# Performance work log

Hardware: AMD Instinct MI355X
Metric: run time of the kernel (lower is better)

## Reference

```python
import jax, jax.numpy as jnp
import numpy as np


def setup_inputs() -> dict:
    key = jax.random.key(0)
    k1, = jax.random.split(key, 1)
    x = jax.random.normal(k1, (8, 256, 128, 128), dtype=jnp.float32)
    alpha = jnp.ones((1,), dtype=jnp.float32)
    return {"x": x, "alpha": alpha}


def reference(x, alpha):
    B, C, H, W = x.shape
    v = x.reshape(B, C, H * W)                 # [B, C, HW] (query=key=value)
    energy = jnp.einsum('bcs,bds->bcd', v, v)  # [B, C, C]
    # max-softmax: softmax(max(energy) - energy) along last dim
    energy_new = jnp.max(energy, axis=-1, keepdims=True) - energy
    w = jax.nn.softmax(energy_new, axis=-1)    # [B, C, C]
    y = jnp.einsum('bcd,bds->bcs', w, v)       # [B, C, HW]
    y = y.reshape(B, C, H, W)
    return alpha * y + x
```

## Files before the change

### kernel.cpp

```cpp
#include <hip/hip_runtime.h>
#include <math.h>

static constexpr int Bn = 8;
static constexpr int Cn = 256;
static constexpr int Sn = 16384;

typedef __bf16 bf16x4 __attribute__((ext_vector_type(4)));
typedef __bf16 bf16x8 __attribute__((ext_vector_type(8)));
typedef float  f32x4  __attribute__((ext_vector_type(4)));

static constexpr int TILE   = 128;
static constexpr int KB     = 32;
static constexpr int KSPLIT = 16;
static constexpr int KSLICE = Sn / KSPLIT;

__device__ __forceinline__ void split_store(__bf16* __restrict__ Hi, __bf16* __restrict__ Lo,
                                            int row, int kq, float4 v) {
  __bf16 h0 = (__bf16)v.x, h1 = (__bf16)v.y, h2 = (__bf16)v.z, h3 = (__bf16)v.w;
  int off = row * 32 + (((kq >> 1) ^ (row & 3)) << 3) + ((kq & 1) << 2);
  *(bf16x4*)&Hi[off] = (bf16x4){h0, h1, h2, h3};
  *(bf16x4*)&Lo[off] = (bf16x4){(__bf16)(v.x - (float)h0), (__bf16)(v.y - (float)h1),
                                (__bf16)(v.z - (float)h2), (__bf16)(v.w - (float)h3)};
}

__device__ __forceinline__ bf16x8 frag_ld(const __bf16* __restrict__ P, int row, int quad) {
  return *(const bf16x8*)&P[row * 32 + ((quad ^ (row & 3)) << 3)];
}

__global__ __launch_bounds__(256, 2) void gram_part_kernel(const float* __restrict__ x,
                                                           float* __restrict__ P) {
  const int b    = blockIdx.z;
  const int tsel = blockIdx.y;
  const int kk   = blockIdx.x;
  const int ti   = (tsel == 1) ? 1 : 0;
  const int tj   = (tsel == 0) ? 0 : 1;
  const bool diag = (tsel < 2);

  const float* vb    = x + (size_t)b * Cn * Sn;
  const float* Abase = vb + (size_t)(ti * TILE) * Sn + kk * KSLICE;
  const float* Bbase = vb + (size_t)(tj * TILE) * Sn + kk * KSLICE;

  __shared__ __align__(16) __bf16 Ah[TILE * 32];
  __shared__ __align__(16) __bf16 Al[TILE * 32];
  __shared__ __align__(16) __bf16 Bh[TILE * 32];
  __shared__ __align__(16) __bf16 Bl[TILE * 32];

  const int t    = threadIdx.x;
  const int lane = t & 63;
  const int wv   = t >> 6;
  const int wr   = wv >> 1;
  const int wc   = wv & 1;
  const int ln   = lane & 15;
  const int quad = lane >> 4;
  const int srow = t >> 3;
  const int skq  = t & 7;

  float4 areg[4], breg[4];
#pragma unroll
  for (int it = 0; it < 4; it++)
    areg[it] = *(const float4*)(Abase + (size_t)(srow + it * 32) * Sn + skq * 4);
  if (!diag) {
#pragma unroll
    for (int it = 0; it < 4; it++)
      breg[it] = *(const float4*)(Bbase + (size_t)(srow + it * 32) * Sn + skq * 4);
  }

  f32x4 acc[4][4];
#pragma unroll
  for (int i = 0; i < 4; i++)
#pragma unroll
    for (int j = 0; j < 4; j++) acc[i][j] = (f32x4){0.f, 0.f, 0.f, 0.f};

  for (int kc = 0; kc < KSLICE; kc += KB) {
#pragma unroll
    for (int it = 0; it < 4; it++) split_store(Ah, Al, srow + it * 32, skq, areg[it]);
    if (!diag) {
#pragma unroll
      for (int it = 0; it < 4; it++) split_store(Bh, Bl, srow + it * 32, skq, breg[it]);
    }
    __syncthreads();

    const __bf16* PH = diag ? Ah : Bh;
    const __bf16* PL = diag ? Al : Bl;

    bf16x8 fah[4], fal[4];
#pragma unroll
    for (int i = 0; i < 4; i++) {
      int ar = wr * 64 + i * 16 + ln;
      fah[i] = frag_ld(Ah, ar, quad);
      fal[i] = frag_ld(Al, ar, quad);
    }

    if (kc + KB < KSLICE) {
#pragma unroll
      for (int it = 0; it < 4; it++)
        areg[it] = *(const float4*)(Abase + (size_t)(srow + it * 32) * Sn + (kc + KB) + skq * 4);
      if (!diag) {
#pragma unroll
        for (int it = 0; it < 4; it++)
          breg[it] = *(const float4*)(Bbase + (size_t)(srow + it * 32) * Sn + (kc + KB) + skq * 4);
      }
    }

#pragma unroll
    for (int j = 0; j < 4; j++) {
      int br = wc * 64 + j * 16 + ln;
      bf16x8 fbh = frag_ld(PH, br, quad);
      bf16x8 fbl = frag_ld(PL, br, quad);
#pragma unroll
      for (int i = 0; i < 4; i++) {
        acc[i][j] = __builtin_amdgcn_mfma_f32_16x16x32_bf16(fah[i], fbh, acc[i][j], 0, 0, 0);
        acc[i][j] = __builtin_amdgcn_mfma_f32_16x16x32_bf16(fah[i], fbl, acc[i][j], 0, 0, 0);
        acc[i][j] = __builtin_amdgcn_mfma_f32_16x16x32_bf16(fal[i], fbh, acc[i][j], 0, 0, 0);
      }
    }
    __syncthreads();
  }

  float* Pb = P + ((size_t)kk * Bn + b) * (Cn * Cn);
#pragma unroll
  for (int i = 0; i < 4; i++)
#pragma unroll
    for (int j = 0; j < 4; j++) {
      int c0 = ti * TILE + wr * 64 + i * 16 + quad * 4;
      int d  = tj * TILE + wc * 64 + j * 16 + ln;
#pragma unroll
      for (int r = 0; r < 4; r++) {
        float v = acc[i][j][r];
        Pb[(size_t)(c0 + r) * Cn + d] = v;
        if (!diag) Pb[(size_t)d * Cn + (c0 + r)] = v;
      }
    }
}

__global__ __launch_bounds__(256) void softmax_reduce_kernel(const float* __restrict__ P,
                                                             float* __restrict__ w) {
  const int wv   = threadIdx.x >> 6;
  const int lane = threadIdx.x & 63;
  const int row  = blockIdx.x * 4 + wv;
  const size_t off = (size_t)row * Cn + lane * 4;

  float4 e = (float4){0.f, 0.f, 0.f, 0.f};
#pragma unroll
  for (int kk = 0; kk < KSPLIT; kk++) {
    float4 p = *(const float4*)&P[(size_t)kk * (Bn * Cn * Cn) + off];
    e.x += p.x; e.y += p.y; e.z += p.z; e.w += p.w;
  }

  float m = fminf(fminf(e.x, e.y), fminf(e.z, e.w));
#pragma unroll
  for (int o = 32; o > 0; o >>= 1) m = fminf(m, __shfl_xor(m, o));

  float4 p;
  p.x = expf(m - e.x); p.y = expf(m - e.y);
  p.z = expf(m - e.z); p.w = expf(m - e.w);
  float s = p.x + p.y + p.z + p.w;
#pragma unroll
  for (int o = 32; o > 0; o >>= 1) s += __shfl_xor(s, o);

  float inv = 1.f / s;
  p.x *= inv; p.y *= inv; p.z *= inv; p.w *= inv;
  *(float4*)&w[off] = p;
}

__global__ __launch_bounds__(256, 2) void ygemm_mfma_kernel(const float* __restrict__ w,
                                                            const float* __restrict__ x,
                                                            const float* __restrict__ alpha,
                                                            float* __restrict__ out) {
  const int b  = blockIdx.z;
  const int m0 = blockIdx.y * 128;
  const int s0 = blockIdx.x * 128;

  const float* Wb = w + ((size_t)b * Cn + m0) * Cn;
  const float* Vb = x + (size_t)b * Cn * Sn;

  __shared__ __align__(16) __bf16 Ah[128 * 32];
  __shared__ __align__(16) __bf16 Al[128 * 32];
  __shared__ __align__(16) __bf16 Bh[128 * 32];
  __shared__ __align__(16) __bf16 Bl[128 * 32];

  const int t    = threadIdx.x;
  const int lane = t & 63;
  const int wv   = t >> 6;
  const int wr   = wv >> 1;
  const int wc   = wv & 1;
  const int ln   = lane & 15;
  const int quad = lane >> 4;
  const int srow = t >> 3;
  const int skq  = t & 7;

  float4 areg[4];
  float  breg[16];

#pragma unroll
  for (int it = 0; it < 4; it++)
    areg[it] = *(const float4*)(Wb + (size_t)(srow + it * 32) * Cn + skq * 4);
#pragma unroll
  for (int it = 0; it < 4; it++) {
    const float* col = Vb + (size_t)(skq * 4) * Sn + s0 + srow + it * 32;
    breg[it * 4 + 0] = col[0];
    breg[it * 4 + 1] = col[(size_t)Sn];
    breg[it * 4 + 2] = col[(size_t)2 * Sn];
    breg[it * 4 + 3] = col[(size_t)3 * Sn];
  }

  f32x4 acc[4][4];
#pragma unroll
  for (int i = 0; i < 4; i++)
#pragma unroll
    for (int j = 0; j < 4; j++) acc[i][j] = (f32x4){0.f, 0.f, 0.f, 0.f};

  for (int kc = 0; kc < Cn; kc += KB) {
#pragma unroll
    for (int it = 0; it < 4; it++) split_store(Ah, Al, srow + it * 32, skq, areg[it]);
#pragma unroll
    for (int it = 0; it < 4; it++) {
      float4 bv = make_float4(breg[it * 4 + 0], breg[it * 4 + 1],
                              breg[it * 4 + 2], breg[it * 4 + 3]);
      split_store(Bh, Bl, srow + it * 32, skq, bv);
    }
    __syncthreads();

    bf16x8 fah[4], fal[4];
#pragma unroll
    for (int i = 0; i < 4; i++) {
      int ar = wr * 64 + i * 16 + ln;
      fah[i] = frag_ld(Ah, ar, quad);
      fal[i] = frag_ld(Al, ar, quad);
    }

    if (kc + KB < Cn) {
#pragma unroll
      for (int it = 0; it < 4; it++)
        areg[it] = *(const float4*)(Wb + (size_t)(srow + it * 32) * Cn + (kc + KB) + skq * 4);
#pragma unroll
      for (int it = 0; it < 4; it++) {
        const float* col = Vb + (size_t)((kc + KB) + skq * 4) * Sn + s0 + srow + it * 32;
        breg[it * 4 + 0] = col[0];
        breg[it * 4 + 1] = col[(size_t)Sn];
        breg[it * 4 + 2] = col[(size_t)2 * Sn];
        breg[it * 4 + 3] = col[(size_t)3 * Sn];
      }
    }

#pragma unroll
    for (int j = 0; j < 4; j++) {
      int br = wc * 64 + j * 16 + ln;
      bf16x8 fbh = frag_ld(Bh, br, quad);
      bf16x8 fbl = frag_ld(Bl, br, quad);
#pragma unroll
      for (int i = 0; i < 4; i++) {
        acc[i][j] = __builtin_amdgcn_mfma_f32_16x16x32_bf16(fah[i], fbh, acc[i][j], 0, 0, 0);
        acc[i][j] = __builtin_amdgcn_mfma_f32_16x16x32_bf16(fah[i], fbl, acc[i][j], 0, 0, 0);
        acc[i][j] = __builtin_amdgcn_mfma_f32_16x16x32_bf16(fal[i], fbh, acc[i][j], 0, 0, 0);
      }
    }
    __syncthreads();
  }

  const float al = alpha[0];
#pragma unroll
  for (int i = 0; i < 4; i++)
#pragma unroll
    for (int j = 0; j < 4; j++) {
      int c = m0 + wr * 64 + i * 16 + quad * 4;
      int s = s0 + wc * 64 + j * 16 + ln;
      const float* xr = x   + ((size_t)b * Cn + c) * Sn + s;
      float*       op = out + ((size_t)b * Cn + c) * Sn + s;
#pragma unroll
      for (int r = 0; r < 4; r++)
        op[(size_t)r * Sn] = al * acc[i][j][r] + xr[(size_t)r * Sn];
    }
}

__global__ __launch_bounds__(256, 2) void gram_atomic_kernel(const float* __restrict__ x,
                                                             float* __restrict__ energy) {
  const int b    = blockIdx.z;
  const int tsel = blockIdx.y;
  const int kk   = blockIdx.x;
  const int ti   = (tsel == 1) ? 1 : 0;
  const int tj   = (tsel == 0) ? 0 : 1;
  const bool diag = (tsel < 2);

  const float* vb    = x + (size_t)b * Cn * Sn;
  const float* Abase = vb + (size_t)(ti * TILE) * Sn + kk * KSLICE;
  const float* Bbase = vb + (size_t)(tj * TILE) * Sn + kk * KSLICE;

  __shared__ __align__(16) __bf16 Ah[TILE * 32];
  __shared__ __align__(16) __bf16 Al[TILE * 32];
  __shared__ __align__(16) __bf16 Bh[TILE * 32];
  __shared__ __align__(16) __bf16 Bl[TILE * 32];

  const int t    = threadIdx.x;
  const int lane = t & 63;
  const int wv   = t >> 6;
  const int wr   = wv >> 1;
  const int wc   = wv & 1;
  const int ln   = lane & 15;
  const int quad = lane >> 4;
  const int srow = t >> 3;
  const int skq  = t & 7;

  float4 areg[4], breg[4];
#pragma unroll
  for (int it = 0; it < 4; it++)
    areg[it] = *(const float4*)(Abase + (size_t)(srow + it * 32) * Sn + skq * 4);
  if (!diag) {
#pragma unroll
    for (int it = 0; it < 4; it++)
      breg[it] = *(const float4*)(Bbase + (size_t)(srow + it * 32) * Sn + skq * 4);
  }

  f32x4 acc[4][4];
#pragma unroll
  for (int i = 0; i < 4; i++)
#pragma unroll
    for (int j = 0; j < 4; j++) acc[i][j] = (f32x4){0.f, 0.f, 0.f, 0.f};

  for (int kc = 0; kc < KSLICE; kc += KB) {
#pragma unroll
    for (int it = 0; it < 4; it++) split_store(Ah, Al, srow + it * 32, skq, areg[it]);
    if (!diag) {
#pragma unroll
      for (int it = 0; it < 4; it++) split_store(Bh, Bl, srow + it * 32, skq, breg[it]);
    }
    __syncthreads();

    const __bf16* PH = diag ? Ah : Bh;
    const __bf16* PL = diag ? Al : Bl;

    bf16x8 fah[4], fal[4];
#pragma unroll
    for (int i = 0; i < 4; i++) {
      int ar = wr * 64 + i * 16 + ln;
      fah[i] = frag_ld(Ah, ar, quad);
      fal[i] = frag_ld(Al, ar, quad);
    }

    if (kc + KB < KSLICE) {
#pragma unroll
      for (int it = 0; it < 4; it++)
        areg[it] = *(const float4*)(Abase + (size_t)(srow + it * 32) * Sn + (kc + KB) + skq * 4);
      if (!diag) {
#pragma unroll
        for (int it = 0; it < 4; it++)
          breg[it] = *(const float4*)(Bbase + (size_t)(srow + it * 32) * Sn + (kc + KB) + skq * 4);
      }
    }

#pragma unroll
    for (int j = 0; j < 4; j++) {
      int br = wc * 64 + j * 16 + ln;
      bf16x8 fbh = frag_ld(PH, br, quad);
      bf16x8 fbl = frag_ld(PL, br, quad);
#pragma unroll
      for (int i = 0; i < 4; i++) {
        acc[i][j] = __builtin_amdgcn_mfma_f32_16x16x32_bf16(fah[i], fbh, acc[i][j], 0, 0, 0);
        acc[i][j] = __builtin_amdgcn_mfma_f32_16x16x32_bf16(fah[i], fbl, acc[i][j], 0, 0, 0);
        acc[i][j] = __builtin_amdgcn_mfma_f32_16x16x32_bf16(fal[i], fbh, acc[i][j], 0, 0, 0);
      }
    }
    __syncthreads();
  }

  float* E = energy + (size_t)b * Cn * Cn;
#pragma unroll
  for (int i = 0; i < 4; i++)
#pragma unroll
    for (int j = 0; j < 4; j++) {
      int c0 = ti * TILE + wr * 64 + i * 16 + quad * 4;
      int d  = tj * TILE + wc * 64 + j * 16 + ln;
#pragma unroll
      for (int r = 0; r < 4; r++) {
        float v = acc[i][j][r];
        atomicAdd(&E[(size_t)(c0 + r) * Cn + d], v);
        if (tsel == 2) atomicAdd(&E[(size_t)d * Cn + (c0 + r)], v);
      }
    }
}

__global__ __launch_bounds__(256) void softmax_kernel(float* __restrict__ energy) {
  const int wv   = threadIdx.x >> 6;
  const int lane = threadIdx.x & 63;
  const int row  = blockIdx.x * 4 + wv;

  float4 e = *(const float4*)&energy[(size_t)row * Cn + lane * 4];
  float m = fminf(fminf(e.x, e.y), fminf(e.z, e.w));
#pragma unroll
  for (int o = 32; o > 0; o >>= 1) m = fminf(m, __shfl_xor(m, o));

  float4 p;
  p.x = expf(m - e.x); p.y = expf(m - e.y);
  p.z = expf(m - e.z); p.w = expf(m - e.w);
  float s = p.x + p.y + p.z + p.w;
#pragma unroll
  for (int o = 32; o > 0; o >>= 1) s += __shfl_xor(s, o);

  float inv = 1.f / s;
  p.x *= inv; p.y *= inv; p.z *= inv; p.w *= inv;
  *(float4*)&energy[(size_t)row * Cn + lane * 4] = p;
}

extern "C" void kernel_launch(void* const* d_in, const int* in_sizes, int n_in,
                              void* d_out, int out_size, void* d_ws, size_t ws_size,
                              hipStream_t stream) {
  const float* x     = (const float*)d_in[0];
  const float* alpha = (const float*)d_in[1];
  float*       out   = (float*)d_out;

  const size_t ecnt  = (size_t)Bn * Cn * Cn;
  const size_t pcnt  = (size_t)KSPLIT * ecnt;
  const size_t need  = (pcnt + ecnt) * sizeof(float);

  dim3 g1(KSPLIT, 3, Bn);
  dim3 g3(Sn / 128, Cn / 128, Bn);

  if (ws_size >= need) {
    float* P = (float*)d_ws;
    float* w = (float*)d_ws + pcnt;

    gram_part_kernel<<<g1, 256, 0, stream>>>(x, P);
    softmax_reduce_kernel<<<(Bn * Cn) / 4, 256, 0, stream>>>(P, w);
    ygemm_mfma_kernel<<<g3, 256, 0, stream>>>(w, x, alpha, out);
  } else {
    float* energy = (float*)d_ws;
    hipMemsetAsync(energy, 0, ecnt * sizeof(float), stream);
    gram_atomic_kernel<<<g1, 256, 0, stream>>>(x, energy);
    softmax_kernel<<<(Bn * Cn) / 4, 256, 0, stream>>>(energy);
    ygemm_mfma_kernel<<<g3, 256, 0, stream>>>(energy, x, alpha, out);
  }
}
```

Baseline: 332.0 us.

## Double-buffer global prefetch registers in gram and y GEMMs with lighter barriers

Reworks the main loops of the gram and output GEMM kernels so global loads are issued two K-steps ahead, using two register sets and a loop unrolled by two. This gives more time to hide global memory latency. Plain __syncthreads is replaced by an LDS-only waitcnt plus s_barrier, so the barrier does not wait on outstanding global loads. The cost is higher register pressure from the second prefetch set, which could lower occupancy or cause spills under launch_bounds(256,2).

```diff
diff --git a/kernel.cpp b/kernel.cpp
--- a/kernel.cpp
+++ b/kernel.cpp
@@ -25,6 +25,65 @@
 
 __device__ __forceinline__ bf16x8 frag_ld(const __bf16* __restrict__ P, int row, int quad) {
   return *(const bf16x8*)&P[row * 32 + ((quad ^ (row & 3)) << 3)];
+}
+
+__device__ __forceinline__ void lds_barrier() {
+  asm volatile("s_waitcnt lgkmcnt(0)" ::: "memory");
+  __builtin_amdgcn_s_barrier();
+}
+
+__device__ __forceinline__ f32x4 mfma16(bf16x8 a, bf16x8 b, f32x4 c) {
+  return __builtin_amdgcn_mfma_f32_16x16x32_bf16(a, b, c, 0, 0, 0);
+}
+
+__device__ __forceinline__ void gram_gload(const float* __restrict__ Abase,
+                                           const float* __restrict__ Bbase,
+                                           bool diag, int srow, int skq, int kc,
+                                           float4 (&ar)[4], float4 (&br)[4]) {
+#pragma unroll
+  for (int it = 0; it < 4; it++)
+    ar[it] = *(const float4*)(Abase + (size_t)(srow + it * 32) * Sn + kc + skq * 4);
+  if (!diag) {
+#pragma unroll
+    for (int it = 0; it < 4; it++)
+      br[it] = *(const float4*)(Bbase + (size_t)(srow + it * 32) * Sn + kc + skq * 4);
+  }
+}
+
+__device__ __forceinline__ void gram_stage(__bf16* Ah, __bf16* Al, __bf16* Bh, __bf16* Bl,
+                                           bool diag, int srow, int skq,
+                                           const float4 (&ar)[4], const float4 (&br)[4]) {
+#pragma unroll
+  for (int it = 0; it < 4; it++) split_store(Ah, Al, srow + it * 32, skq, ar[it]);
+  if (!diag) {
+#pragma unroll
+    for (int it = 0; it < 4; it++) split_store(Bh, Bl, srow + it * 32, skq, br[it]);
+  }
+}
+
+__device__ __forceinline__ void tile_mfma(const __bf16* Ah, const __bf16* Al,
+                                          const __bf16* PH, const __bf16* PL,
+                                          int wr, int wc, int ln, int quad,
+                                          f32x4 (&acc)[4][4]) {
+  bf16x8 fah[4], fal[4];
+#pragma unroll
+  for (int i = 0; i < 4; i++) {
+    int ar = wr * 64 + i * 16 + ln;
+    fah[i] = frag_ld(Ah, ar, quad);
+    fal[i] = frag_ld(Al, ar, quad);
+  }
+#pragma unroll
+  for (int j = 0; j < 4; j++) {
+    int br = wc * 64 + j * 16 + ln;
+    bf16x8 fbh = frag_ld(PH, br, quad);
+    bf16x8 fbl = frag_ld(PL, br, quad);
+#pragma unroll
+    for (int i = 0; i < 4; i++) {
+      acc[i][j] = mfma16(fah[i], fbh, acc[i][j]);
+      acc[i][j] = mfma16(fah[i], fbl, acc[i][j]);
+      acc[i][j] = mfma16(fal[i], fbh, acc[i][j]);
+    }
+  }
 }
 
 __global__ __launch_bounds__(256, 2) void gram_part_kernel(const float* __restrict__ x,
@@ -55,15 +114,15 @@
   const int srow = t >> 3;
   const int skq  = t & 7;
 
-  float4 areg[4], breg[4];
-#pragma unroll
-  for (int it = 0; it < 4; it++)
-    areg[it] = *(const float4*)(Abase + (size_t)(srow + it * 32) * Sn + skq * 4);
-  if (!diag) {
-#pragma unroll
-    for (int it = 0; it < 4; it++)
-      breg[it] = *(const float4*)(Bbase + (size_t)(srow + it * 32) * Sn + skq * 4);
-  }
+  const __bf16* PH = diag ? Ah : Bh;
+  const __bf16* PL = diag ? Al : Bl;
+
+  float4 arA[4], brA[4], arB[4], brB[4];
+
+  gram_gload(Abase, Bbase, diag, srow, skq, 0, arA, brA);
+  gram_gload(Abase, Bbase, diag, srow, skq, KB, arB, brB);
+  gram_stage(Ah, Al, Bh, Bl, diag, srow, skq, arA, brA);
+  lds_barrier();
 
   f32x4 acc[4][4];
 #pragma unroll
@@ -71,50 +130,22 @@
 #pragma unroll
     for (int j = 0; j < 4; j++) acc[i][j] = (f32x4){0.f, 0.f, 0.f, 0.f};
 
-  for (int kc = 0; kc < KSLICE; kc += KB) {
-#pragma unroll
-    for (int it = 0; it < 4; it++) split_store(Ah, Al, srow + it * 32, skq, areg[it]);
-    if (!diag) {
-#pragma unroll
-      for (int it = 0; it < 4; it++) split_store(Bh, Bl, srow + it * 32, skq, breg[it]);
-    }
-    __syncthreads();
-
-    const __bf16* PH = diag ? Ah : Bh;
-    const __bf16* PL = diag ? Al : Bl;
-
-    bf16x8 fah[4], fal[4];
-#pragma unroll
-    for (int i = 0; i < 4; i++) {
-      int ar = wr * 64 + i * 16 + ln;
-      fah[i] = frag_ld(Ah, ar, quad);
-      fal[i] = frag_ld(Al, ar, quad);
-    }
-
-    if (kc + KB < KSLICE) {
-#pragma unroll
-      for (int it = 0; it < 4; it++)
-        areg[it] = *(const float4*)(Abase + (size_t)(srow + it * 32) * Sn + (kc + KB) + skq * 4);
-      if (!diag) {
-#pragma unroll
-        for (int it = 0; it < 4; it++)
-          breg[it] = *(const float4*)(Bbase + (size_t)(srow + it * 32) * Sn + (kc + KB) + skq * 4);
-      }
-    }
-
-#pragma unroll
-    for (int j = 0; j < 4; j++) {
-      int br = wc * 64 + j * 16 + ln;
-      bf16x8 fbh = frag_ld(PH, br, quad);
-      bf16x8 fbl = frag_ld(PL, br, quad);
-#pragma unroll
-      for (int i = 0; i < 4; i++) {
-        acc[i][j] = __builtin_amdgcn_mfma_f32_16x16x32_bf16(fah[i], fbh, acc[i][j], 0, 0, 0);
-        acc[i][j] = __builtin_amdgcn_mfma_f32_16x16x32_bf16(fah[i], fbl, acc[i][j], 0, 0, 0);
-        acc[i][j] = __builtin_amdgcn_mfma_f32_16x16x32_bf16(fal[i], fbh, acc[i][j], 0, 0, 0);
-      }
-    }
-    __syncthreads();
+  for (int kc = 0; kc < KSLICE; kc += 2 * KB) {
+    if (kc + 2 * KB < KSLICE)
+      gram_gload(Abase, Bbase, diag, srow, skq, kc + 2 * KB, arA, brA);
+    tile_mfma(Ah, Al, PH, PL, wr, wc, ln, quad, acc);
+    lds_barrier();
+    gram_stage(Ah, Al, Bh, Bl, diag, srow, skq, arB, brB);
+    lds_barrier();
+
+    const int c1 = kc + KB;
+    if (c1 + 2 * KB < KSLICE)
+      gram_gload(Abase, Bbase, diag, srow, skq, c1 + 2 * KB, arB, brB);
+    tile_mfma(Ah, Al, PH, PL, wr, wc, ln, quad, acc);
+    lds_barrier();
+    if (c1 + KB < KSLICE)
+      gram_stage(Ah, Al, Bh, Bl, diag, srow, skq, arA, brA);
+    lds_barrier();
   }
 
   float* Pb = P + ((size_t)kk * Bn + b) * (Cn * Cn);
@@ -161,6 +192,36 @@
   float inv = 1.f / s;
   p.x *= inv; p.y *= inv; p.z *= inv; p.w *= inv;
   *(float4*)&w[off] = p;
+}
+
+__device__ __forceinline__ void y_gload(const float* __restrict__ Wb,
+                                        const float* __restrict__ Vb, int s0,
+                                        int srow, int skq, int kc,
+                                        float4 (&ar)[4], float (&br)[16]) {
+#pragma unroll
+  for (int it = 0; it < 4; it++)
+    ar[it] = *(const float4*)(Wb + (size_t)(srow + it * 32) * Cn + kc + skq * 4);
+#pragma unroll
+  for (int it = 0; it < 4; it++) {
+    const float* col = Vb + (size_t)(kc + skq * 4) * Sn + s0 + srow + it * 32;
+    br[it * 4 + 0] = col[0];
+    br[it * 4 + 1] = col[(size_t)Sn];
+    br[it * 4 + 2] = col[(size_t)2 * Sn];
+    br[it * 4 + 3] = col[(size_t)3 * Sn];
+  }
+}
+
+__device__ __forceinline__ void y_stage(__bf16* Ah, __bf16* Al, __bf16* Bh, __bf16* Bl,
+                                        int srow, int skq,
+                                        const float4 (&ar)[4], const float (&br)[16]) {
+#pragma unroll
+  for (int it = 0; it < 4; it++) split_store(Ah, Al, srow + it * 32, skq, ar[it]);
+#pragma unroll
+  for (int it = 0; it < 4; it++) {
+    float4 bv = make_float4(br[it * 4 + 0], br[it * 4 + 1],
+                            br[it * 4 + 2], br[it * 4 + 3]);
+    split_store(Bh, Bl, srow + it * 32, skq, bv);
+  }
 }
 
 __global__ __launch_bounds__(256, 2) void ygemm_mfma_kernel(const float* __restrict__ w,
@@ -189,20 +250,13 @@
   const int srow = t >> 3;
   const int skq  = t & 7;
 
-  float4 areg[4];
-  float  breg[16];
-
-#pragma unroll
-  for (int it = 0; it < 4; it++)
-    areg[it] = *(const float4*)(Wb + (size_t)(srow + it * 32) * Cn + skq * 4);
-#pragma unroll
-  for (int it = 0; it < 4; it++) {
-    const float* col = Vb + (size_t)(skq * 4) * Sn + s0 + srow + it * 32;
-    breg[it * 4 + 0] = col[0];
-    breg[it * 4 + 1] = col[(size_t)Sn];
-    breg[it * 4 + 2] = col[(size_t)2 * Sn];
-    breg[it * 4 + 3] = col[(size_t)3 * Sn];
-  }
+  float4 arA[4], arB[4];
+  float  brA[16], brB[16];
+
+  y_gload(Wb, Vb, s0, srow, skq, 0, arA, brA);
+  y_gload(Wb, Vb, s0, srow, skq, KB, arB, brB);
+  y_stage(Ah, Al, Bh, Bl, srow, skq, arA, brA);
+  lds_barrier();
 
   f32x4 acc[4][4];
 #pragma unroll
@@ -210,52 +264,22 @@
 #pragma unroll
     for (int j = 0; j < 4; j++) acc[i][j] = (f32x4){0.f, 0.f, 0.f, 0.f};
 
-  for (int kc = 0; kc < Cn; kc += KB) {
-#pragma unroll
-    for (int it = 0; it < 4; it++) split_store(Ah, Al, srow + it * 32, skq, areg[it]);
-#pragma unroll
-    for (int it = 0; it < 4; it++) {
-      float4 bv = make_float4(breg[it * 4 + 0], breg[it * 4 + 1],
-                              breg[it * 4 + 2], breg[it * 4 + 3]);
-      split_store(Bh, Bl, srow + it * 32, skq, bv);
-    }
-    __syncthreads();
-
-    bf16x8 fah[4], fal[4];
-#pragma unroll
-    for (int i = 0; i < 4; i++) {
-      int ar = wr * 64 + i * 16 + ln;
-      fah[i] = frag_ld(Ah, ar, quad);
-      fal[i] = frag_ld(Al, ar, quad);
-    }
-
-    if (kc + KB < Cn) {
-#pragma unroll
-      for (int it = 0; it < 4; it++)
-        areg[it] = *(const float4*)(Wb + (size_t)(srow + it * 32) * Cn + (kc + KB) + skq * 4);
-#pragma unroll
-      for (int it = 0; it < 4; it++) {
-        const float* col = Vb + (size_t)((kc + KB) + skq * 4) * Sn + s0 + srow + it * 32;
-        breg[it * 4 + 0] = col[0];
-        breg[it * 4 + 1] = col[(size_t)Sn];
-        breg[it * 4 + 2] = col[(size_t)2 * Sn];
-        breg[it * 4 + 3] = col[(size_t)3 * Sn];
-      }
-    }
-
-#pragma unroll
-    for (int j = 0; j < 4; j++) {
-      int br = wc * 64 + j * 16 + ln;
-      bf16x8 fbh = frag_ld(Bh, br, quad);
-      bf16x8 fbl = frag_ld(Bl, br, quad);
-#pragma unroll
-      for (int i = 0; i < 4; i++) {
-        acc[i][j] = __builtin_amdgcn_mfma_f32_16x16x32_bf16(fah[i], fbh, acc[i][j], 0, 0, 0);
-        acc[i][j] = __builtin_amdgcn_mfma_f32_16x16x32_bf16(fah[i], fbl, acc[i][j], 0, 0, 0);
-        acc[i][j] = __builtin_amdgcn_mfma_f32_16x16x32_bf16(fal[i], fbh, acc[i][j], 0, 0, 0);
-      }
-    }
-    __syncthreads();
+  for (int kc = 0; kc < Cn; kc += 2 * KB) {
+    if (kc + 2 * KB < Cn)
+      y_gload(Wb, Vb, s0, srow, skq, kc + 2 * KB, arA, brA);
+    tile_mfma(Ah, Al, Bh, Bl, wr, wc, ln, quad, acc);
+    lds_barrier();
+    y_stage(Ah, Al, Bh, Bl, srow, skq, arB, brB);
+    lds_barrier();
+
+    const int c1 = kc + KB;
+    if (c1 + 2 * KB < Cn)
+      y_gload(Wb, Vb, s0, srow, skq, c1 + 2 * KB, arB, brB);
+    tile_mfma(Ah, Al, Bh, Bl, wr, wc, ln, quad, acc);
+    lds_barrier();
+    if (c1 + KB < Cn)
+      y_stage(Ah, Al, Bh, Bl, srow, skq, arA, brA);
+    lds_barrier();
   }
 
   const float al = alpha[0];
@@ -329,14 +353,6 @@
     const __bf16* PH = diag ? Ah : Bh;
     const __bf16* PL = diag ? Al : Bl;
 
-    bf16x8 fah[4], fal[4];
-#pragma unroll
-    for (int i = 0; i < 4; i++) {
-      int ar = wr * 64 + i * 16 + ln;
-      fah[i] = frag_ld(Ah, ar, quad);
-      fal[i] = frag_ld(Al, ar, quad);
-    }
-
     if (kc + KB < KSLICE) {
 #pragma unroll
       for (int it = 0; it < 4; it++)
@@ -348,18 +364,7 @@
       }
     }
 
-#pragma unroll
-    for (int j = 0; j < 4; j++) {
-      int br = wc * 64 + j * 16 + ln;
-      bf16x8 fbh = frag_ld(PH, br, quad);
-      bf16x8 fbl = frag_ld(PL, br, quad);
-#pragma unroll
-      for (int i = 0; i < 4; i++) {
-        acc[i][j] = __builtin_amdgcn_mfma_f32_16x16x32_bf16(fah[i], fbh, acc[i][j], 0, 0, 0);
-        acc[i][j] = __builtin_amdgcn_mfma_f32_16x16x32_bf16(fah[i], fbl, acc[i][j], 0, 0, 0);
-        acc[i][j] = __builtin_amdgcn_mfma_f32_16x16x32_bf16(fal[i], fbh, acc[i][j], 0, 0, 0);
-      }
-    }
+    tile_mfma(Ah, Al, PH, PL, wr, wc, ln, quad, acc);
     __syncthreads();
   }
 
```

Result: slower. 354.1 us (+6.7%).
